# Performance work log

Measured on AMD Instinct MI355X. Metric: run time of the kernel, lower is better.

## Reference

```python
import jax, jax.numpy as jnp
import numpy as np

N_NEAR = 16
BN_EPS = 1e-5


def fps(xyz, n_center):
    # farthest point sampling, deterministic start at index 0. xyz: [B,N,C]
    B, N, _ = xyz.shape
    dist0 = jnp.full((B, N), jnp.inf, dtype=xyz.dtype)
    far0 = jnp.zeros((B,), dtype=jnp.int32)

    def step(carry, _):
        dist, far = carry
        centroid = jnp.take_along_axis(xyz, far[:, None, None], axis=1)  # [B,1,C]
        d = jnp.sum((xyz - centroid) ** 2, axis=-1)                       # [B,N]
        dist = jnp.minimum(dist, d)
        nxt = jnp.argmax(dist, axis=-1).astype(jnp.int32)
        return (dist, nxt), far

    _, idxs = jax.lax.scan(step, (dist0, far0), None, length=n_center)
    return jnp.transpose(idxs)  # [B, n_center]


def knn(xyz, k):
    # k nearest neighbors (self included), xyz: [B,N,C] -> idx [B,N,k]
    sq = jnp.sum(xyz * xyz, axis=-1)
    d = sq[:, :, None] - 2.0 * jnp.einsum('bnc,bmc->bnm', xyz, xyz) + sq[:, None, :]
    _, idx = jax.lax.top_k(-d, k)
    return idx


def gather_points(x, idx):
    # x: [B,N,...], idx: [B,*dims] int -> [B,*dims,...]
    return jax.vmap(lambda xb, ib: xb[ib])(x, idx)


def conv_bn_relu(x, W, b, g, be):
    # x: [B,C,K,S]; 1x1 Conv2d + BatchNorm2d (training/batch stats) + ReLU
    y = jnp.einsum('oc,bcks->boks', W, x) + b[None, :, None, None]
    mean = jnp.mean(y, axis=(0, 2, 3), keepdims=True)
    var = jnp.mean((y - mean) ** 2, axis=(0, 2, 3), keepdims=True)  # biased var, as torch BN
    y = (y - mean) * jax.lax.rsqrt(var + BN_EPS)
    y = y * g[None, :, None, None] + be[None, :, None, None]
    return jax.nn.relu(y)


def setup_inputs() -> dict:
    key = jax.random.key(0)
    ks = jax.random.split(key, 8)
    B, N, EMB = 16, 2048, 64
    mlp = [64, 128, 256]
    in_ch = 2 + EMB
    inp = {
        'xy': jax.random.normal(ks[0], (B, 2, N), dtype=jnp.float32),
        'fea': jax.random.normal(ks[1], (B, EMB, N), dtype=jnp.float32),
    }
    last = in_ch
    for i, out in enumerate(mlp):
        inp[f'W{i+1}'] = 0.1 * jax.random.normal(ks[2 + i], (out, last), dtype=jnp.float32)
        inp[f'b{i+1}'] = jnp.zeros((out,), dtype=jnp.float32)
        inp[f'g{i+1}'] = jnp.ones((out,), dtype=jnp.float32)
        inp[f'be{i+1}'] = jnp.zeros((out,), dtype=jnp.float32)
        last = out
    return inp


def reference(xy, fea, W1, b1, g1, be1, W2, b2, g2, be2, W3, b3, g3, be3):
    B, _, N = xy.shape
    n_center = N // 2 + 1
    xyz = jnp.transpose(xy, (0, 2, 1))   # [B,N,2]
    f = jnp.transpose(fea, (0, 2, 1))    # [B,N,emb]

    fps_idx = fps(xyz, n_center)                      # [B,S]
    new_xyz = gather_points(xyz, fps_idx)             # [B,S,2]
    knn_idx = knn(xyz, N_NEAR)                        # [B,N,k]
    knn_of_fps = gather_points(knn_idx, fps_idx)      # [B,S,k]
    grouped_xyz = gather_points(xyz, knn_of_fps)      # [B,S,k,2]
    grouped_norm = grouped_xyz - new_xyz[:, :, None, :]
    grouped_f = gather_points(f, knn_of_fps)          # [B,S,k,emb]
    new_fea = jnp.concatenate([grouped_norm, grouped_f], axis=-1)  # [B,S,k,C]

    x = jnp.transpose(new_fea, (0, 3, 2, 1))          # [B,C,k,S]
    for (W, b, g, be) in ((W1, b1, g1, be1), (W2, b2, g2, be2), (W3, b3, g3, be3)):
        x = conv_bn_relu(x, W, b, g, be)
    out = jnp.max(x, axis=2)                          # [B,C_out,S]
    return jnp.transpose(new_xyz, (0, 2, 1)), out
```

## Files before the change

kernel.cpp:

```cpp
#include <hip/hip_runtime.h>
#include <math.h>

#define B_   16
#define N_   2048
#define S_   1025
#define K_   16
#define EMB_ 64
#define NF_  (B_ * S_ * K_)
#define NCH_ (NF_ / 64)
#define NBS_ (NCH_ * 4)

typedef float v2f __attribute__((ext_vector_type(2)));
typedef short bf16x8 __attribute__((ext_vector_type(8)));
typedef float f32x4 __attribute__((ext_vector_type(4)));

__device__ __forceinline__ unsigned short f2bf(float f) {
  unsigned u = __float_as_uint(f);
  u += 0x7fffu + ((u >> 16) & 1u);
  return (unsigned short)(u >> 16);
}
__device__ __forceinline__ float bfl(unsigned pk) { return __uint_as_float((pk & 0xffffu) << 16); }
__device__ __forceinline__ float bfh(unsigned pk) { return __uint_as_float(pk & 0xffff0000u); }

__global__ __launch_bounds__(256) __attribute__((amdgpu_waves_per_eu(1, 1)))
void fps_pk_kernel(const float* __restrict__ xy, const float* __restrict__ fea,
                   const float* __restrict__ W1,
                   const float* __restrict__ W2, const float* __restrict__ W3,
                   int* __restrict__ fps_idx, float* __restrict__ new_xyz,
                   float* __restrict__ out0, unsigned* __restrict__ Pp,
                   unsigned short* __restrict__ W2b, unsigned short* __restrict__ W3b) {
  __shared__ float smem[8192];
  if (blockIdx.x < 16) {
    const int b = blockIdx.x;
    float2* lxy = reinterpret_cast<float2*>(smem);
    const int lane = threadIdx.x;
    const float* xb = xy + (size_t)b * 2 * N_;
    v2f pxp[16], pyp[16];
    float dist[32];
    if (lane < 64) {
      const float2* xb2 = (const float2*)xb;
      const float2* yb2 = (const float2*)(xb + N_);
#pragma unroll
      for (int q = 0; q < 16; ++q) {
        float2 x01 = xb2[lane * 16 + q];
        float2 y01 = yb2[lane * 16 + q];
        int p = lane * 32 + 2 * q;
        lxy[p] = make_float2(x01.x, y01.x);
        lxy[p + 1] = make_float2(x01.y, y01.y);
        pxp[q][0] = x01.x; pxp[q][1] = x01.y;
        pyp[q][0] = y01.x; pyp[q][1] = y01.y;
        dist[2 * q] = __builtin_inff();
        dist[2 * q + 1] = __builtin_inff();
      }
#pragma unroll
      for (int q = 0; q < 16; ++q) {
        asm volatile("" : "+v"(pxp[q]), "+v"(pyp[q]));
      }
    }
    __syncthreads();
    if (lane < 64) {
      int cur = 0;
      for (int t = 0; t < S_; ++t) {
        float2 c = lxy[cur];
        if (lane == 0) {
          fps_idx[b * S_ + t] = cur;
          new_xyz[(b * S_ + t) * 2 + 0] = c.x;
          new_xyz[(b * S_ + t) * 2 + 1] = c.y;
          out0[b * 2 * S_ + t] = c.x;
          out0[b * 2 * S_ + S_ + t] = c.y;
        }
        const float ncx = -c.x, ncy = -c.y;
        v2f ncx2; ncx2[0] = ncx; ncx2[1] = ncx;
        v2f ncy2; ncy2[0] = ncy; ncy2[1] = ncy;
#pragma unroll
        for (int q = 0; q < 16; ++q) {
          v2f dx, dy, sx, sy, dd;
          asm("v_pk_add_f32 %0, %1, %2" : "=v"(dx) : "v"(pxp[q]), "v"(ncx2));
          asm("v_pk_add_f32 %0, %1, %2" : "=v"(dy) : "v"(pyp[q]), "v"(ncy2));
          asm("v_pk_mul_f32 %0, %1, %1" : "=v"(sx) : "v"(dx));
          asm("v_pk_mul_f32 %0, %1, %1" : "=v"(sy) : "v"(dy));
          asm("v_pk_add_f32 %0, %1, %2" : "=v"(dd) : "v"(sx), "v"(sy));
          dist[2 * q] = fminf(dist[2 * q], dd[0]);
          dist[2 * q + 1] = fminf(dist[2 * q + 1], dd[1]);
        }
        float m1[16], m2[8], m3[4], m4[2];
#pragma unroll
        for (int j = 0; j < 16; ++j) m1[j] = fmaxf(dist[2 * j], dist[2 * j + 1]);
#pragma unroll
        for (int j = 0; j < 8; ++j) m2[j] = fmaxf(m1[2 * j], m1[2 * j + 1]);
#pragma unroll
        for (int j = 0; j < 4; ++j) m3[j] = fmaxf(m2[2 * j], m2[2 * j + 1]);
        m4[0] = fmaxf(m3[0], m3[1]);
        m4[1] = fmaxf(m3[2], m3[3]);
        const float lmax = fmaxf(m4[0], m4[1]);
        int xr = __float_as_int(lmax);
#define DPP_MAX_STEP(CTRL)                                                        \
        {                                                                         \
          int tmp_ = __builtin_amdgcn_update_dpp(xr, xr, (CTRL), 0xF, 0xF, false);\
          xr = __float_as_int(fmaxf(__int_as_float(xr), __int_as_float(tmp_)));   \
        }
        DPP_MAX_STEP(0x111)
        DPP_MAX_STEP(0x112)
        DPP_MAX_STEP(0x114)
        DPP_MAX_STEP(0x118)
        DPP_MAX_STEP(0x142)
        DPP_MAX_STEP(0x143)
#undef DPP_MAX_STEP
        const float g = __int_as_float(__builtin_amdgcn_readlane(xr, 63));
        int n = (m4[0] == g) ? 0 : 1;
        float c3 = (n & 1) ? m3[2] : m3[0];
        n = 2 * n + ((c3 == g) ? 0 : 1);
        float lo2 = (n & 1) ? m2[2] : m2[0];
        float hi2 = (n & 1) ? m2[6] : m2[4];
        float c2 = (n & 2) ? hi2 : lo2;
        n = 2 * n + ((c2 == g) ? 0 : 1);
        float a0 = (n & 1) ? m1[2] : m1[0];
        float a1 = (n & 1) ? m1[6] : m1[4];
        float a2 = (n & 1) ? m1[10] : m1[8];
        float a3 = (n & 1) ? m1[14] : m1[12];
        float b0 = (n & 2) ? a1 : a0;
        float b1 = (n & 2) ? a3 : a2;
        float c1 = (n & 4) ? b1 : b0;
        n = 2 * n + ((c1 == g) ? 0 : 1);
        float e0 = (n & 1) ? dist[2] : dist[0];
        float e1 = (n & 1) ? dist[6] : dist[4];
        float e2 = (n & 1) ? dist[10] : dist[8];
        float e3 = (n & 1) ? dist[14] : dist[12];
        float e4 = (n & 1) ? dist[18] : dist[16];
        float e5 = (n & 1) ? dist[22] : dist[20];
        float e6 = (n & 1) ? dist[26] : dist[24];
        float e7 = (n & 1) ? dist[30] : dist[28];
        float f0 = (n & 2) ? e1 : e0;
        float f1 = (n & 2) ? e3 : e2;
        float f2 = (n & 2) ? e5 : e4;
        float f3 = (n & 2) ? e7 : e6;
        float g0 = (n & 4) ? f1 : f0;
        float g1 = (n & 4) ? f3 : f2;
        float c0 = (n & 8) ? g1 : g0;
        const int lf = 2 * n + ((c0 == g) ? 0 : 1);
        unsigned long long mask = __ballot(lmax == g);
        int first = __ffsll(mask) - 1;
        cur = __builtin_amdgcn_readlane(lane * 32 + lf, first);
      }
    }
  } else if (blockIdx.x < 528) {
    const int bid = blockIdx.x - 16;
    const int t = threadIdx.x;
    const int b = bid >> 5;
    const int pt0 = (bid & 31) << 6;
    float* W1L = smem;
    float* feaL = smem + 4096;
#pragma unroll
    for (int p = 0; p < 16; ++p) {
      int idx = t + 256 * p;
      int c = idx >> 6, e = idx & 63;
      W1L[e * 64 + c] = W1[c * 66 + 2 + e];
      int r = (t >> 6) + 4 * p, cc = t & 63;
      feaL[r * 64 + cc] = fea[((size_t)b * 64 + r) * N_ + pt0 + cc];
    }
    __syncthreads();
    const int tpt = t & 15, tcq = t >> 4;
    float acc[4][4];
#pragma unroll
    for (int i = 0; i < 4; ++i)
#pragma unroll
      for (int j = 0; j < 4; ++j) acc[i][j] = 0.f;
    for (int e = 0; e < 64; ++e) {
      float4 a4 = *reinterpret_cast<const float4*>(&W1L[e * 64 + tcq * 4]);
      float4 b4 = *reinterpret_cast<const float4*>(&feaL[e * 64 + tpt * 4]);
      const float av[4] = {a4.x, a4.y, a4.z, a4.w};
      const float bvv[4] = {b4.x, b4.y, b4.z, b4.w};
#pragma unroll
      for (int i = 0; i < 4; ++i)
#pragma unroll
        for (int j = 0; j < 4; ++j) acc[i][j] = fmaf(av[i], bvv[j], acc[i][j]);
    }
#pragma unroll
    for (int j = 0; j < 4; ++j) {
      int pt = tpt * 4 + j;
      unsigned lo = (unsigned)f2bf(acc[0][j]) | ((unsigned)f2bf(acc[1][j]) << 16);
      unsigned hi = (unsigned)f2bf(acc[2][j]) | ((unsigned)f2bf(acc[3][j]) << 16);
      unsigned* dst = &Pp[((size_t)(b * N_ + pt0 + pt)) * 32 + tcq * 2];
      dst[0] = lo;
      dst[1] = hi;
    }
  } else {
    const int t = threadIdx.x;
    for (int i = t; i < 128 * 64; i += 256) W2b[i] = f2bf(W2[i]);
    for (int i = t; i < 256 * 128; i += 256) W3b[i] = f2bf(W3[i]);
  }
}

__global__ __launch_bounds__(256) void knn_kernel(const float* __restrict__ xy,
                                                  const int* __restrict__ fps_idx,
                                                  int* __restrict__ knn_sel) {
  const int b = blockIdx.y;
  __shared__ float2 lxy[N_];
  __shared__ double lsq[N_];
  const float* xb = xy + (size_t)b * 2 * N_;
  for (int p = threadIdx.x; p < N_; p += 256) {
    float x = xb[p], y = xb[N_ + p];
    lxy[p] = make_float2(x, y);
    lsq[p] = (double)x * (double)x + (double)y * (double)y;
  }
  __syncthreads();
  const int t = threadIdx.x;
  const int s = blockIdx.x * 8 + (t >> 5);
  if (s >= S_) return;
  const int oct = t & 31;
  const int p0 = fps_idx[b * S_ + s];
  float2 q = lxy[p0];
  const double xn = (double)q.x, yn = (double)q.y;
  const double sqn = lsq[p0];
  double d16[16];
  int i16[16];
#pragma unroll
  for (int j = 0; j < 16; ++j) { d16[j] = __builtin_inf(); i16[j] = 0x7fffffff; }
  const int mlo = oct * 64;
  for (int m0 = mlo; m0 < mlo + 64; m0 += 4) {
    double dd[4];
#pragma unroll
    for (int u = 0; u < 4; ++u) {
      float2 p = lxy[m0 + u];
      double dot = (double)p.x * xn + (double)p.y * yn;
      dd[u] = (sqn - 2.0 * dot) + lsq[m0 + u];
    }
#pragma unroll
    for (int u = 0; u < 4; ++u) {
      if (dd[u] < d16[15]) {
        double d = dd[u];
        int mi = m0 + u;
#pragma unroll
        for (int j = 15; j >= 1; --j) {
          bool shift = d < d16[j - 1];
          bool ins = d < d16[j];
          d16[j] = shift ? d16[j - 1] : (ins ? d : d16[j]);
          i16[j] = shift ? i16[j - 1] : (ins ? mi : i16[j]);
        }
        if (d < d16[0]) { d16[0] = d; i16[0] = mi; }
      }
    }
  }
#pragma unroll
  for (int w = 1; w <= 16; w <<= 1) {
    double nd[16]; int ni[16];
#pragma unroll
    for (int i = 0; i < 16; ++i) {
      double rd = __shfl_xor(d16[15 - i], w, 64);
      int ri = __shfl_xor(i16[15 - i], w, 64);
      bool takeR = (rd < d16[i]) || (rd == d16[i] && ri < i16[i]);
      nd[i] = takeR ? rd : d16[i];
      ni[i] = takeR ? ri : i16[i];
    }
#pragma unroll
    for (int i = 0; i < 16; ++i) { d16[i] = nd[i]; i16[i] = ni[i]; }
    if (w < 16) {
#pragma unroll
      for (int dstg = 8; dstg >= 1; dstg >>= 1) {
#pragma unroll
        for (int i = 0; i < 16; ++i) {
          if ((i & dstg) == 0) {
            int a = i, c = i + dstg;
            bool sw = (d16[a] > d16[c]) || (d16[a] == d16[c] && i16[a] > i16[c]);
            double tlo = sw ? d16[c] : d16[a];
            double thi = sw ? d16[a] : d16[c];
            int ulo = sw ? i16[c] : i16[a];
            int uhi = sw ? i16[a] : i16[c];
            d16[a] = tlo; d16[c] = thi; i16[a] = ulo; i16[c] = uhi;
          }
        }
      }
    }
  }
  if (oct == 0) {
    int* dst = knn_sel + ((size_t)b * S_ + s) * K_;
#pragma unroll
    for (int j = 0; j < 16; ++j) dst[j] = i16[j];
  }
}

__global__ __launch_bounds__(256) void yk1_kernel(const float* __restrict__ xy,
                                                  const int* __restrict__ knn_sel,
                                                  const float* __restrict__ new_xyz,
                                                  const unsigned* __restrict__ Pp,
                                                  const float* __restrict__ W1,
                                                  const float* __restrict__ b1,
                                                  unsigned* __restrict__ Y1p) {
  __shared__ float w0s[64], w1s[64], bbs[64];
  const int t = threadIdx.x;
  if (t < 64) { w0s[t] = W1[t * 66 + 0]; w1s[t] = W1[t * 66 + 1]; bbs[t] = b1[t]; }
  __syncthreads();
  const int n = blockIdx.x * 256 + t;
  const int bs = n >> 4;
  const int b = bs / S_;
  const int nbr = knn_sel[n];
  const float dx = xy[(size_t)b * 2 * N_ + nbr] - new_xyz[bs * 2 + 0];
  const float dy = xy[(size_t)b * 2 * N_ + N_ + nbr] - new_xyz[bs * 2 + 1];
  const unsigned* prow = &Pp[((size_t)(b * N_ + nbr)) * 32];
#pragma unroll 8
  for (int j = 0; j < 32; ++j) {
    unsigned pj = prow[j];
    int c = 2 * j;
    float v0 = bfl(pj) + w0s[c] * dx + w1s[c] * dy + bbs[c];
    float v1 = bfh(pj) + w0s[c + 1] * dx + w1s[c + 1] * dy + bbs[c + 1];
    Y1p[(size_t)j * NF_ + n] = (unsigned)f2bf(v0) | ((unsigned)f2bf(v1) << 16);
  }
}

__global__ __launch_bounds__(256) void rowstats_kernel(const unsigned* __restrict__ Y1p,
                                                       float* __restrict__ parts) {
  const int j = blockIdx.x & 31;
  const int seg = blockIdx.x >> 5;
  const int SEG = NF_ / 8;
  const unsigned* p = Y1p + (size_t)j * NF_ + (size_t)seg * SEG;
  double s0 = 0, q0 = 0, s1 = 0, q1 = 0;
  for (int i = threadIdx.x; i < SEG; i += 256) {
    unsigned pk = p[i];
    double a = (double)bfl(pk), b = (double)bfh(pk);
    s0 += a; q0 = fma(a, a, q0);
    s1 += b; q1 = fma(b, b, q1);
  }
  __shared__ double sh[4][256];
  sh[0][threadIdx.x] = s0; sh[1][threadIdx.x] = q0;
  sh[2][threadIdx.x] = s1; sh[3][threadIdx.x] = q1;
  __syncthreads();
  for (int o = 128; o > 0; o >>= 1) {
    if (threadIdx.x < o) {
#pragma unroll
      for (int u = 0; u < 4; ++u) sh[u][threadIdx.x] += sh[u][threadIdx.x + o];
    }
    __syncthreads();
  }
  if (threadIdx.x == 0) {
    float* dst = parts + (size_t)(j * 8 + seg) * 4;
    dst[0] = (float)sh[0][0];
    dst[1] = (float)sh[2][0];
    dst[2] = (float)sh[1][0];
    dst[3] = (float)sh[3][0];
  }
}

__global__ void redabsch1_kernel(const float* __restrict__ parts,
                                 const float* __restrict__ g, const float* __restrict__ be,
                                 float* __restrict__ A, float* __restrict__ D) {
  int m = threadIdx.x;
  if (m >= 64) return;
  int j = m >> 1, par = m & 1;
  double a = 0.0, b = 0.0;
  for (int seg = 0; seg < 8; ++seg) {
    const float* src = parts + (size_t)(j * 8 + seg) * 4;
    a += (double)src[par];
    b += (double)src[2 + par];
  }
  double mu = a * (1.0 / NF_);
  double var = b * (1.0 / NF_) - mu * mu;
  double aa = (double)g[m] / sqrt(var + 1e-5);
  A[m] = (float)aa;
  D[m] = (float)((double)be[m] - aa * mu);
}

__global__ void redabsch_kernel(const float* __restrict__ parts, int P, int M,
                                const float* __restrict__ g, const float* __restrict__ be,
                                float* __restrict__ A, float* __restrict__ D) {
  int m = threadIdx.x;
  if (m >= M) return;
  double a = 0.0, b = 0.0;
  for (int p = 0; p < P; ++p) {
    a += (double)parts[(size_t)p * 2 * M + m];
    b += (double)parts[(size_t)p * 2 * M + M + m];
  }
  double mu = a * (1.0 / NF_);
  double var = b * (1.0 / NF_) - mu * mu;
  double aa = (double)g[m] / sqrt(var + 1e-5);
  A[m] = (float)aa;
  D[m] = (float)((double)be[m] - aa * mu);
}

__device__ __forceinline__ float rowsum16(float v) {
#define RADD(CTRL) { int tm_ = __builtin_amdgcn_update_dpp(0, __float_as_int(v), (CTRL), 0xF, 0xF, true); \
                     v += __int_as_float(tm_); }
  RADD(0x111) RADD(0x112) RADD(0x114) RADD(0x118)
#undef RADD
  return v;
}

__device__ __forceinline__ void stage_x1(const unsigned* Y1p, const float* ab1, char* x1c,
                                         size_t n0, int w, int L) {
#pragma unroll
  for (int e = 0; e < 8; ++e) {
    int k0 = 2 * (w + 4 * e);
    unsigned pkv = Y1p[(size_t)(k0 >> 1) * NF_ + n0 + L];
    float v0 = fmaxf(fmaf(bfl(pkv), ab1[k0], ab1[64 + k0]), 0.f);
    float v1 = fmaxf(fmaf(bfh(pkv), ab1[k0 + 1], ab1[64 + k0 + 1]), 0.f);
    unsigned pk = (unsigned)f2bf(v0) | ((unsigned)f2bf(v1) << 16);
    *reinterpret_cast<unsigned*>(&x1c[L * 128 + ((2 * k0) ^ ((L & 7) << 4))]) = pk;
  }
}

__global__ __launch_bounds__(256) void passA_mfma_kernel(
    const unsigned* __restrict__ Y1p, const unsigned short* __restrict__ W2b,
    const float* __restrict__ A1v, const float* __restrict__ Bc1v,
    float* __restrict__ parts) {
  __shared__ float ab1[128];
  __shared__ __align__(16) unsigned short x1b[64 * 64];
  const int t = threadIdx.x;
  const int w = t >> 6, L = t & 63;
  if (t < 128) ab1[t] = (t < 64) ? A1v[t] : Bc1v[t - 64];
  bf16x8 w2f[2][2];
#pragma unroll
  for (int rb = 0; rb < 2; ++rb)
#pragma unroll
    for (int ks = 0; ks < 2; ++ks) {
      int row = (2 * w + rb) * 16 + (L & 15);
      int koff = ks * 32 + (L >> 4) * 8;
      w2f[rb][ks] = *reinterpret_cast<const bf16x8*>(&W2b[row * 64 + koff]);
    }
  float vs[2][4], vq[2][4];
#pragma unroll
  for (int rb = 0; rb < 2; ++rb)
#pragma unroll
    for (int r = 0; r < 4; ++r) { vs[rb][r] = 0.f; vq[rb][r] = 0.f; }
  char* x1c = reinterpret_cast<char*>(x1b);
  for (int ch = blockIdx.x; ch < NCH_; ch += 512) {
    const size_t n0 = (size_t)ch * 64;
    __syncthreads();
    stage_x1(Y1p, ab1, x1c, n0, w, L);
    __syncthreads();
#pragma unroll
    for (int rb = 0; rb < 2; ++rb) {
      f32x4 acc2[4];
#pragma unroll
      for (int cb = 0; cb < 4; ++cb) acc2[cb][0] = acc2[cb][1] = acc2[cb][2] = acc2[cb][3] = 0.f;
#pragma unroll
      for (int ks = 0; ks < 2; ++ks)
#pragma unroll
        for (int cb = 0; cb < 4; ++cb) {
          int n = cb * 16 + (L & 15);
          int koff = ks * 32 + (L >> 4) * 8;
          bf16x8 bfr = *reinterpret_cast<const bf16x8*>(&x1c[n * 128 + ((2 * koff) ^ ((n & 7) << 4))]);
          acc2[cb] = __builtin_amdgcn_mfma_f32_16x16x32_bf16(w2f[rb][ks], bfr, acc2[cb], 0, 0, 0);
        }
#pragma unroll
      for (int cb = 0; cb < 4; ++cb)
#pragma unroll
        for (int r = 0; r < 4; ++r) {
          float y = acc2[cb][r];
          vs[rb][r] += y;
          vq[rb][r] = fmaf(y, y, vq[rb][r]);
        }
    }
  }
#pragma unroll
  for (int rb = 0; rb < 2; ++rb)
#pragma unroll
    for (int r = 0; r < 4; ++r) {
      float s = rowsum16(vs[rb][r]);
      float q = rowsum16(vq[rb][r]);
      if ((L & 15) == 15) {
        int row = (2 * w + rb) * 16 + (L >> 4) * 4 + r;
        parts[(size_t)blockIdx.x * 256 + row] = s;
        parts[(size_t)blockIdx.x * 256 + 128 + row] = q;
      }
    }
}

__global__ __launch_bounds__(256) void passB_mfma_kernel(
    const unsigned* __restrict__ Y1p,
    const unsigned short* __restrict__ W2b, const unsigned short* __restrict__ W3b,
    const float* __restrict__ A1v, const float* __restrict__ Bc1v,
    const float* __restrict__ A2v, const float* __restrict__ D2v,
    float* __restrict__ parts, unsigned* __restrict__ M3) {
  __shared__ float ab1[128];
  __shared__ __align__(16) unsigned short x1b[64 * 64];
  __shared__ __align__(16) unsigned short x2b[64 * 128];
  const int t = threadIdx.x;
  const int w = t >> 6, L = t & 63;
  if (t < 128) ab1[t] = (t < 64) ? A1v[t] : Bc1v[t - 64];
  bf16x8 w3f[4][4];
#pragma unroll
  for (int rb = 0; rb < 4; ++rb)
#pragma unroll
    for (int ks = 0; ks < 4; ++ks) {
      int row = (4 * w + rb) * 16 + (L & 15);
      int koff = ks * 32 + (L >> 4) * 8;
      w3f[rb][ks] = *reinterpret_cast<const bf16x8*>(&W3b[row * 128 + koff]);
    }
  bf16x8 w2f[2][2];
#pragma unroll
  for (int rb = 0; rb < 2; ++rb)
#pragma unroll
    for (int ks = 0; ks < 2; ++ks) {
      int row = (2 * w + rb) * 16 + (L & 15);
      int koff = ks * 32 + (L >> 4) * 8;
      w2f[rb][ks] = *reinterpret_cast<const bf16x8*>(&W2b[row * 64 + koff]);
    }
  float vs[4][4], vq[4][4];
#pragma unroll
  for (int rb = 0; rb < 4; ++rb)
#pragma unroll
    for (int r = 0; r < 4; ++r) { vs[rb][r] = 0.f; vq[rb][r] = 0.f; }
  char* x1c = reinterpret_cast<char*>(x1b);
  char* x2c = reinterpret_cast<char*>(x2b);
  for (int ch = blockIdx.x; ch < NCH_; ch += 256) {
    const size_t n0 = (size_t)ch * 64;
    __syncthreads();
    stage_x1(Y1p, ab1, x1c, n0, w, L);
    __syncthreads();
#pragma unroll
    for (int rb = 0; rb < 2; ++rb) {
      f32x4 acc2[4];
#pragma unroll
      for (int cb = 0; cb < 4; ++cb) acc2[cb][0] = acc2[cb][1] = acc2[cb][2] = acc2[cb][3] = 0.f;
#pragma unroll
      for (int ks = 0; ks < 2; ++ks)
#pragma unroll
        for (int cb = 0; cb < 4; ++cb) {
          int n = cb * 16 + (L & 15);
          int koff = ks * 32 + (L >> 4) * 8;
          bf16x8 bfr = *reinterpret_cast<const bf16x8*>(&x1c[n * 128 + ((2 * koff) ^ ((n & 7) << 4))]);
          acc2[cb] = __builtin_amdgcn_mfma_f32_16x16x32_bf16(w2f[rb][ks], bfr, acc2[cb], 0, 0, 0);
        }
#pragma unroll
      for (int cb = 0; cb < 4; ++cb) {
        int n = cb * 16 + (L & 15);
        int kbase = (2 * w + rb) * 16 + (L >> 4) * 4;
#pragma unroll
        for (int rp = 0; rp < 2; ++rp) {
          int r0 = 2 * rp;
          float a0 = A2v[kbase + r0], d0 = D2v[kbase + r0];
          float a1 = A2v[kbase + r0 + 1], d1 = D2v[kbase + r0 + 1];
          float v0 = fmaxf(fmaf(acc2[cb][r0], a0, d0), 0.f);
          float v1 = fmaxf(fmaf(acc2[cb][r0 + 1], a1, d1), 0.f);
          unsigned pk = (unsigned)f2bf(v0) | ((unsigned)f2bf(v1) << 16);
          int k0 = kbase + r0;
          *reinterpret_cast<unsigned*>(&x2c[n * 256 + ((2 * k0) ^ ((n & 7) << 4))]) = pk;
        }
      }
    }
    __syncthreads();
    bf16x8 b3[4][4];
#pragma unroll
    for (int cb = 0; cb < 4; ++cb)
#pragma unroll
      for (int ks = 0; ks < 4; ++ks) {
        int n = cb * 16 + (L & 15);
        int koff = ks * 32 + (L >> 4) * 8;
        b3[cb][ks] = *reinterpret_cast<const bf16x8*>(&x2c[n * 256 + ((2 * koff) ^ ((n & 7) << 4))]);
      }
#pragma unroll
    for (int rb = 0; rb < 4; ++rb) {
      f32x4 acc3[4];
#pragma unroll
      for (int cb = 0; cb < 4; ++cb) acc3[cb][0] = acc3[cb][1] = acc3[cb][2] = acc3[cb][3] = 0.f;
#pragma unroll
      for (int ks = 0; ks < 4; ++ks)
#pragma unroll
        for (int cb = 0; cb < 4; ++cb)
          acc3[cb] = __builtin_amdgcn_mfma_f32_16x16x32_bf16(w3f[rb][ks], b3[cb][ks], acc3[cb], 0, 0, 0);
#pragma unroll
      for (int cb = 0; cb < 4; ++cb)
#pragma unroll
        for (int r = 0; r < 4; ++r) {
          float y = acc3[cb][r];
          vs[rb][r] += y;
          vq[rb][r] = fmaf(y, y, vq[rb][r]);
        }
      {
        int rowbase = (4 * w + rb) * 16 + (L >> 4) * 4;
#pragma unroll
        for (int cb = 0; cb < 4; ++cb) {
#pragma unroll
          for (int r = 0; r < 4; ++r) {
            float v = acc3[cb][r];
            int xi = __float_as_int(v), xm = __float_as_int(v);
#define RMAX(CTRL) { int tm_ = __builtin_amdgcn_update_dpp(xi, xi, (CTRL), 0xF, 0xF, false); \
                     xi = __float_as_int(fmaxf(__int_as_float(xi), __int_as_float(tm_))); }
#define RMIN(CTRL) { int tm_ = __builtin_amdgcn_update_dpp(xm, xm, (CTRL), 0xF, 0xF, false); \
                     xm = __float_as_int(fminf(__int_as_float(xm), __int_as_float(tm_))); }
            RMAX(0x111) RMAX(0x112) RMAX(0x114) RMAX(0x118)
            RMIN(0x111) RMIN(0x112) RMIN(0x114) RMIN(0x118)
#undef RMAX
#undef RMIN
            if ((L & 15) == 15) {
              int row = rowbase + r;
              int bs = ch * 4 + cb;
              M3[(size_t)row * NBS_ + bs] =
                  (unsigned)f2bf(__int_as_float(xi)) | ((unsigned)f2bf(__int_as_float(xm)) << 16);
            }
          }
        }
      }
    }
  }
#pragma unroll
  for (int rb = 0; rb < 4; ++rb)
#pragma unroll
    for (int r = 0; r < 4; ++r) {
      float s = rowsum16(vs[rb][r]);
      float q = rowsum16(vq[rb][r]);
      if ((L & 15) == 15) {
        int row = (4 * w + rb) * 16 + (L >> 4) * 4 + r;
        parts[(size_t)blockIdx.x * 512 + row] = s;
        parts[(size_t)blockIdx.x * 512 + 256 + row] = q;
      }
    }
}

__global__ __launch_bounds__(256) void final_small_kernel(
    const unsigned* __restrict__ M3, const float* __restrict__ A3,
    const float* __restrict__ D3, float* __restrict__ out1) {
  int gid = blockIdx.x * 256 + threadIdx.x;
  int row = gid / NBS_, bs = gid - row * NBS_;
  unsigned pk = M3[gid];
  float vmax = bfl(pk);
  float vmin = bfh(pk);
  float a = A3[row];
  float v = (a >= 0.f) ? vmax : vmin;
  int b = bs / S_, s = bs - b * S_;
  out1[((size_t)(b * 256 + row)) * S_ + s] = fmaxf(fmaf(v, a, D3[row]), 0.f);
}

__global__ void diag_kernel(float* out, float v) {
  if (threadIdx.x == 0 && blockIdx.x == 0) out[0] = v;
}

extern "C" void kernel_launch(void* const* d_in, const int* in_sizes, int n_in,
                              void* d_out, int out_size, void* d_ws, size_t ws_size,
                              hipStream_t stream) {
  const float* xy  = (const float*)d_in[0];
  const float* fea = (const float*)d_in[1];
  const float* W1  = (const float*)d_in[2];
  const float* b1  = (const float*)d_in[3];
  const float* g1  = (const float*)d_in[4];
  const float* be1 = (const float*)d_in[5];
  const float* W2  = (const float*)d_in[6];
  const float* g2  = (const float*)d_in[8];
  const float* be2 = (const float*)d_in[9];
  const float* W3  = (const float*)d_in[10];
  const float* g3  = (const float*)d_in[12];
  const float* be3 = (const float*)d_in[13];
  float* out = (float*)d_out;
  float* out1 = out + B_ * 2 * S_;

  char* w = (char*)d_ws;
  size_t off = 0;
  auto take = [&](size_t bytes) -> void* {
    void* p = w + off;
    off += (bytes + 255) & ~(size_t)255;
    return p;
  };
  int*      fps_idx = (int*)take((size_t)B_ * S_ * 4);
  float*    new_xyz = (float*)take((size_t)B_ * S_ * 2 * 4);
  int*      knn_sel = (int*)take((size_t)NF_ * 4);
  unsigned* Pp      = (unsigned*)take((size_t)B_ * N_ * 32 * 4);
  unsigned* Y1p     = (unsigned*)take((size_t)32 * NF_ * 4);
  float*    parts1  = (float*)take((size_t)256 * 4 * 4);
  float*    A1      = (float*)take(64 * 4);
  float*    Bc1     = (float*)take(64 * 4);
  float*    partsA  = (float*)take((size_t)512 * 256 * 4);
  float*    A2      = (float*)take(128 * 4);
  float*    D2      = (float*)take(128 * 4);
  float*    partsB  = (float*)take((size_t)256 * 512 * 4);
  float*    A3      = (float*)take(256 * 4);
  float*    D3      = (float*)take(256 * 4);
  unsigned short* W2b = (unsigned short*)take((size_t)128 * 64 * 2);
  unsigned short* W3b = (unsigned short*)take((size_t)256 * 128 * 2);
  unsigned* M3      = (unsigned*)take((size_t)256 * NBS_ * 4);

  if (off > ws_size) {
    diag_kernel<<<1, 64, 0, stream>>>(out, (float)(ws_size >> 20));
    return;
  }

  fps_pk_kernel<<<16 + 512 + 1, 256, 0, stream>>>(xy, fea, W1, W2, W3,
                                                  fps_idx, new_xyz, out, Pp, W2b, W3b);
  knn_kernel<<<dim3((S_ + 7) / 8, B_), 256, 0, stream>>>(xy, fps_idx, knn_sel);
  yk1_kernel<<<NF_ / 256, 256, 0, stream>>>(xy, knn_sel, new_xyz, Pp, W1, b1, Y1p);

  rowstats_kernel<<<256, 256, 0, stream>>>(Y1p, parts1);
  redabsch1_kernel<<<1, 64, 0, stream>>>(parts1, g1, be1, A1, Bc1);

  passA_mfma_kernel<<<512, 256, 0, stream>>>(Y1p, W2b, A1, Bc1, partsA);
  redabsch_kernel<<<1, 128, 0, stream>>>(partsA, 512, 128, g2, be2, A2, D2);

  passB_mfma_kernel<<<256, 256, 0, stream>>>(Y1p, W2b, W3b, A1, Bc1, A2, D2, partsB, M3);
  redabsch_kernel<<<1, 256, 0, stream>>>(partsB, 256, 256, g3, be3, A3, D3);

  final_small_kernel<<<(256 * NBS_) / 256, 256, 0, stream>>>(M3, A3, D3, out1);
}
```

Baseline: 1.351 ms.

## Fuse all stages into one persistent kernel with grid barriers and streamed FPS progress

Replaces the chain of ten separate launches with a single persistent 256-block kernel that uses atomic grid barriers between BN stages. The 16 FPS blocks publish per-batch progress, so the other blocks can pull KNN work items from an atomic queue and start on already-sampled centers while FPS is still running, after first draining the precompute work. This targets launch gaps and the serialization of KNN behind the long FPS loop. The risks are spin-wait overhead, the need for all 256 blocks to be co-resident to avoid deadlock, and reduced parallelism in later stages now capped at 256 blocks.

```diff
diff --git a/kernel.cpp b/kernel.cpp
--- a/kernel.cpp
+++ b/kernel.cpp
@@ -9,10 +9,18 @@
 #define NF_  (B_ * S_ * K_)
 #define NCH_ (NF_ / 64)
 #define NBS_ (NCH_ * 4)
+#define NBLK 256
+#define PK_UNITS 513
+#define KNN_ITEMS (129 * 16)
 
 typedef float v2f __attribute__((ext_vector_type(2)));
 typedef short bf16x8 __attribute__((ext_vector_type(8)));
 typedef float f32x4 __attribute__((ext_vector_type(4)));
+
+#define AL(p)    __hip_atomic_load((p), __ATOMIC_ACQUIRE, __HIP_MEMORY_SCOPE_AGENT)
+#define ALR(p)   __hip_atomic_load((p), __ATOMIC_RELAXED, __HIP_MEMORY_SCOPE_AGENT)
+#define ASR(p,v) __hip_atomic_store((p), (v), __ATOMIC_RELEASE, __HIP_MEMORY_SCOPE_AGENT)
+#define AADD(p)  __hip_atomic_fetch_add((p), 1, __ATOMIC_ACQ_REL, __HIP_MEMORY_SCOPE_AGENT)
 
 __device__ __forceinline__ unsigned short f2bf(float f) {
   unsigned u = __float_as_uint(f);
@@ -22,18 +30,67 @@
 __device__ __forceinline__ float bfl(unsigned pk) { return __uint_as_float((pk & 0xffffu) << 16); }
 __device__ __forceinline__ float bfh(unsigned pk) { return __uint_as_float(pk & 0xffff0000u); }
 
-__global__ __launch_bounds__(256) __attribute__((amdgpu_waves_per_eu(1, 1)))
-void fps_pk_kernel(const float* __restrict__ xy, const float* __restrict__ fea,
-                   const float* __restrict__ W1,
-                   const float* __restrict__ W2, const float* __restrict__ W3,
-                   int* __restrict__ fps_idx, float* __restrict__ new_xyz,
-                   float* __restrict__ out0, unsigned* __restrict__ Pp,
-                   unsigned short* __restrict__ W2b, unsigned short* __restrict__ W3b) {
-  __shared__ float smem[8192];
-  if (blockIdx.x < 16) {
-    const int b = blockIdx.x;
-    float2* lxy = reinterpret_cast<float2*>(smem);
-    const int lane = threadIdx.x;
+__device__ __forceinline__ float rowsum16(float v) {
+#define RADD(CTRL) { int tm_ = __builtin_amdgcn_update_dpp(0, __float_as_int(v), (CTRL), 0xF, 0xF, true); \
+                     v += __int_as_float(tm_); }
+  RADD(0x111) RADD(0x112) RADD(0x114) RADD(0x118)
+#undef RADD
+  return v;
+}
+
+__global__ void diag_kernel(float* out, float v) {
+  if (threadIdx.x == 0 && blockIdx.x == 0) out[0] = v;
+}
+
+__global__ __launch_bounds__(256, 1)
+void mega_kernel(const float* __restrict__ xy, const float* __restrict__ fea,
+                 const float* __restrict__ W1, const float* __restrict__ b1,
+                 const float* __restrict__ g1, const float* __restrict__ be1,
+                 const float* __restrict__ W2, const float* __restrict__ g2,
+                 const float* __restrict__ be2,
+                 const float* __restrict__ W3, const float* __restrict__ g3,
+                 const float* __restrict__ be3,
+                 int* fps_idx, float* new_xyz, int* knn_sel,
+                 unsigned* Pp, unsigned* Y1p, float* parts1,
+                 float* A1, float* Bc1, float* partsA, float* A2, float* D2,
+                 float* partsB, float* A3, float* D3,
+                 unsigned short* W2b, unsigned short* W3b, unsigned* M3,
+                 float* out0, float* out1, int* flags) {
+  __shared__ float2 sh_lxy[N_];
+  __shared__ double sh_lsq[N_];
+  __shared__ float sh_pkA[4096];
+  __shared__ float sh_pkB[4096];
+  __shared__ float sh_w0[64], sh_w1[64], sh_bb[64];
+  __shared__ double sh_red[4][256];
+  __shared__ float sh_ab1[128];
+  __shared__ __align__(16) unsigned short sh_x1b[64 * 64];
+  __shared__ __align__(16) unsigned short sh_x2b[64 * 128];
+  __shared__ int sh_unit;
+  __shared__ int sh_epoch;
+  const int bid = blockIdx.x;
+  const int tid = threadIdx.x;
+  int* progress = flags + 8;
+  if (tid == 0) sh_epoch = 0;
+  __syncthreads();
+
+  auto gbar = [&]() {
+    __syncthreads();
+    if (tid == 0) {
+      int my = ++sh_epoch;
+      int arrived = AADD(&flags[0]);
+      if (arrived == NBLK - 1) {
+        __hip_atomic_store(&flags[0], 0, __ATOMIC_RELAXED, __HIP_MEMORY_SCOPE_AGENT);
+        ASR(&flags[1], my);
+      } else {
+        while (AL(&flags[1]) < my) __builtin_amdgcn_s_sleep(8);
+      }
+    }
+    __syncthreads();
+  };
+
+  if (bid < 16) {
+    const int b = bid;
+    const int lane = tid;
     const float* xb = xy + (size_t)b * 2 * N_;
     v2f pxp[16], pyp[16];
     float dist[32];
@@ -45,8 +102,8 @@
         float2 x01 = xb2[lane * 16 + q];
         float2 y01 = yb2[lane * 16 + q];
         int p = lane * 32 + 2 * q;
-        lxy[p] = make_float2(x01.x, y01.x);
-        lxy[p + 1] = make_float2(x01.y, y01.y);
+        sh_lxy[p] = make_float2(x01.x, y01.x);
+        sh_lxy[p + 1] = make_float2(x01.y, y01.y);
         pxp[q][0] = x01.x; pxp[q][1] = x01.y;
         pyp[q][0] = y01.x; pyp[q][1] = y01.y;
         dist[2 * q] = __builtin_inff();
@@ -61,7 +118,7 @@
     if (lane < 64) {
       int cur = 0;
       for (int t = 0; t < S_; ++t) {
-        float2 c = lxy[cur];
+        float2 c = sh_lxy[cur];
         if (lane == 0) {
           fps_idx[b * S_ + t] = cur;
           new_xyz[(b * S_ + t) * 2 + 0] = c.x;
@@ -115,12 +172,12 @@
         float c2 = (n & 2) ? hi2 : lo2;
         n = 2 * n + ((c2 == g) ? 0 : 1);
         float a0 = (n & 1) ? m1[2] : m1[0];
-        float a1 = (n & 1) ? m1[6] : m1[4];
-        float a2 = (n & 1) ? m1[10] : m1[8];
-        float a3 = (n & 1) ? m1[14] : m1[12];
-        float b0 = (n & 2) ? a1 : a0;
-        float b1 = (n & 2) ? a3 : a2;
-        float c1 = (n & 4) ? b1 : b0;
+        float a1v = (n & 1) ? m1[6] : m1[4];
+        float a2v = (n & 1) ? m1[10] : m1[8];
+        float a3v = (n & 1) ? m1[14] : m1[12];
+        float b0 = (n & 2) ? a1v : a0;
+        float b1v = (n & 2) ? a3v : a2v;
+        float c1 = (n & 4) ? b1v : b0;
         n = 2 * n + ((c1 == g) ? 0 : 1);
         float e0 = (n & 1) ? dist[2] : dist[0];
         float e1 = (n & 1) ? dist[6] : dist[4];
@@ -135,493 +192,489 @@
         float f2 = (n & 2) ? e5 : e4;
         float f3 = (n & 2) ? e7 : e6;
         float g0 = (n & 4) ? f1 : f0;
-        float g1 = (n & 4) ? f3 : f2;
-        float c0 = (n & 8) ? g1 : g0;
+        float g1v = (n & 4) ? f3 : f2;
+        float c0 = (n & 8) ? g1v : g0;
         const int lf = 2 * n + ((c0 == g) ? 0 : 1);
         unsigned long long mask = __ballot(lmax == g);
         int first = __ffsll(mask) - 1;
         cur = __builtin_amdgcn_readlane(lane * 32 + lf, first);
-      }
-    }
-  } else if (blockIdx.x < 528) {
-    const int bid = blockIdx.x - 16;
-    const int t = threadIdx.x;
-    const int b = bid >> 5;
-    const int pt0 = (bid & 31) << 6;
-    float* W1L = smem;
-    float* feaL = smem + 4096;
-#pragma unroll
-    for (int p = 0; p < 16; ++p) {
-      int idx = t + 256 * p;
-      int c = idx >> 6, e = idx & 63;
-      W1L[e * 64 + c] = W1[c * 66 + 2 + e];
-      int r = (t >> 6) + 4 * p, cc = t & 63;
-      feaL[r * 64 + cc] = fea[((size_t)b * 64 + r) * N_ + pt0 + cc];
-    }
+        if (lane == 0 && ((t & 31) == 31 || t == S_ - 1)) {
+          ASR(&progress[b], t + 1);
+        }
+      }
+    }
+  } else {
+    for (;;) {
+      __syncthreads();
+      if (tid == 0) sh_unit = AADD(&flags[2]);
+      __syncthreads();
+      int u = sh_unit;
+      if (u >= PK_UNITS) break;
+      if (u < 512) {
+        const int b = u >> 5;
+        const int pt0 = (u & 31) << 6;
+#pragma unroll
+        for (int p = 0; p < 16; ++p) {
+          int idx = tid + 256 * p;
+          int c = idx >> 6, e = idx & 63;
+          sh_pkA[e * 64 + c] = W1[c * 66 + 2 + e];
+          int r = (tid >> 6) + 4 * p, cc = tid & 63;
+          sh_pkB[r * 64 + cc] = fea[((size_t)b * 64 + r) * N_ + pt0 + cc];
+        }
+        __syncthreads();
+        const int tpt = tid & 15, tcq = tid >> 4;
+        float acc[4][4];
+#pragma unroll
+        for (int i = 0; i < 4; ++i)
+#pragma unroll
+          for (int j = 0; j < 4; ++j) acc[i][j] = 0.f;
+        for (int e = 0; e < 64; ++e) {
+          float4 a4 = *reinterpret_cast<const float4*>(&sh_pkA[e * 64 + tcq * 4]);
+          float4 b4 = *reinterpret_cast<const float4*>(&sh_pkB[e * 64 + tpt * 4]);
+          const float av[4] = {a4.x, a4.y, a4.z, a4.w};
+          const float bvv[4] = {b4.x, b4.y, b4.z, b4.w};
+#pragma unroll
+          for (int i = 0; i < 4; ++i)
+#pragma unroll
+            for (int j = 0; j < 4; ++j) acc[i][j] = fmaf(av[i], bvv[j], acc[i][j]);
+        }
+#pragma unroll
+        for (int j = 0; j < 4; ++j) {
+          int pt = tpt * 4 + j;
+          unsigned lo = (unsigned)f2bf(acc[0][j]) | ((unsigned)f2bf(acc[1][j]) << 16);
+          unsigned hi = (unsigned)f2bf(acc[2][j]) | ((unsigned)f2bf(acc[3][j]) << 16);
+          unsigned* dst = &Pp[((size_t)(b * N_ + pt0 + pt)) * 32 + tcq * 2];
+          dst[0] = lo;
+          dst[1] = hi;
+        }
+      } else {
+        for (int i = tid; i < 128 * 64; i += 256) W2b[i] = f2bf(W2[i]);
+        for (int i = tid; i < 256 * 128; i += 256) W3b[i] = f2bf(W3[i]);
+      }
+    }
+    for (;;) {
+      __syncthreads();
+      if (tid == 0) sh_unit = AADD(&flags[4]);
+      __syncthreads();
+      int it = sh_unit;
+      if (it >= KNN_ITEMS) break;
+      const int b = it & 15;
+      const int s0 = (it >> 4) * 8;
+      const int sHi = (s0 + 8 < S_) ? (s0 + 8) : S_;
+      if (tid == 0) {
+        while (AL(&progress[b]) < sHi) __builtin_amdgcn_s_sleep(8);
+      }
+      __syncthreads();
+      const float* xb = xy + (size_t)b * 2 * N_;
+      for (int p = tid; p < N_; p += 256) {
+        float x = xb[p], y = xb[N_ + p];
+        sh_lxy[p] = make_float2(x, y);
+        sh_lsq[p] = (double)x * (double)x + (double)y * (double)y;
+      }
+      __syncthreads();
+      const int s = s0 + (tid >> 5);
+      const int oct = tid & 31;
+      if (s < S_) {
+        const int p0 = ALR((int*)&fps_idx[b * S_ + s]);
+        float2 q = sh_lxy[p0];
+        const double xn = (double)q.x, yn = (double)q.y;
+        const double sqn = sh_lsq[p0];
+        double d16[16];
+        int i16[16];
+#pragma unroll
+        for (int j = 0; j < 16; ++j) { d16[j] = __builtin_inf(); i16[j] = 0x7fffffff; }
+        const int mlo = oct * 64;
+        for (int m0 = mlo; m0 < mlo + 64; m0 += 4) {
+          double dd[4];
+#pragma unroll
+          for (int u2 = 0; u2 < 4; ++u2) {
+            float2 p = sh_lxy[m0 + u2];
+            double dot = (double)p.x * xn + (double)p.y * yn;
+            dd[u2] = (sqn - 2.0 * dot) + sh_lsq[m0 + u2];
+          }
+#pragma unroll
+          for (int u2 = 0; u2 < 4; ++u2) {
+            if (dd[u2] < d16[15]) {
+              double d = dd[u2];
+              int mi = m0 + u2;
+#pragma unroll
+              for (int j = 15; j >= 1; --j) {
+                bool shift = d < d16[j - 1];
+                bool ins = d < d16[j];
+                d16[j] = shift ? d16[j - 1] : (ins ? d : d16[j]);
+                i16[j] = shift ? i16[j - 1] : (ins ? mi : i16[j]);
+              }
+              if (d < d16[0]) { d16[0] = d; i16[0] = mi; }
+            }
+          }
+        }
+#pragma unroll
+        for (int w = 1; w <= 16; w <<= 1) {
+          double nd[16]; int ni[16];
+#pragma unroll
+          for (int i = 0; i < 16; ++i) {
+            double rd = __shfl_xor(d16[15 - i], w, 64);
+            int ri = __shfl_xor(i16[15 - i], w, 64);
+            bool takeR = (rd < d16[i]) || (rd == d16[i] && ri < i16[i]);
+            nd[i] = takeR ? rd : d16[i];
+            ni[i] = takeR ? ri : i16[i];
+          }
+#pragma unroll
+          for (int i = 0; i < 16; ++i) { d16[i] = nd[i]; i16[i] = ni[i]; }
+          if (w < 16) {
+#pragma unroll
+            for (int dstg = 8; dstg >= 1; dstg >>= 1) {
+#pragma unroll
+              for (int i = 0; i < 16; ++i) {
+                if ((i & dstg) == 0) {
+                  int a = i, c = i + dstg;
+                  bool sw = (d16[a] > d16[c]) || (d16[a] == d16[c] && i16[a] > i16[c]);
+                  double tlo = sw ? d16[c] : d16[a];
+                  double thi = sw ? d16[a] : d16[c];
+                  int ulo = sw ? i16[c] : i16[a];
+                  int uhi = sw ? i16[a] : i16[c];
+                  d16[a] = tlo; d16[c] = thi; i16[a] = ulo; i16[c] = uhi;
+                }
+              }
+            }
+          }
+        }
+        if (oct == 0) {
+          int* dst = knn_sel + ((size_t)b * S_ + s) * K_;
+#pragma unroll
+          for (int j = 0; j < 16; ++j) dst[j] = i16[j];
+        }
+      }
+    }
+  }
+
+  gbar();
+
+  if (tid < 64) { sh_w0[tid] = W1[tid * 66 + 0]; sh_w1[tid] = W1[tid * 66 + 1]; sh_bb[tid] = b1[tid]; }
+  __syncthreads();
+  for (int u = bid; u < NF_ / 256; u += NBLK) {
+    const int n = u * 256 + tid;
+    const int bs = n >> 4;
+    const int b = bs / S_;
+    const int nbr = knn_sel[n];
+    const float dx = xy[(size_t)b * 2 * N_ + nbr] - new_xyz[bs * 2 + 0];
+    const float dy = xy[(size_t)b * 2 * N_ + N_ + nbr] - new_xyz[bs * 2 + 1];
+    const unsigned* prow = &Pp[((size_t)(b * N_ + nbr)) * 32];
+#pragma unroll 8
+    for (int j = 0; j < 32; ++j) {
+      unsigned pj = prow[j];
+      int c = 2 * j;
+      float v0 = bfl(pj) + sh_w0[c] * dx + sh_w1[c] * dy + sh_bb[c];
+      float v1 = bfh(pj) + sh_w0[c + 1] * dx + sh_w1[c + 1] * dy + sh_bb[c + 1];
+      Y1p[(size_t)j * NF_ + n] = (unsigned)f2bf(v0) | ((unsigned)f2bf(v1) << 16);
+    }
+  }
+
+  gbar();
+
+  {
+    const int j = bid & 31;
+    const int seg = bid >> 5;
+    const int SEG = NF_ / 8;
+    const unsigned* p = Y1p + (size_t)j * NF_ + (size_t)seg * SEG;
+    double s0 = 0, q0 = 0, s1 = 0, q1 = 0;
+    for (int i = tid; i < SEG; i += 256) {
+      unsigned pk = p[i];
+      double a = (double)bfl(pk), b2 = (double)bfh(pk);
+      s0 += a; q0 = fma(a, a, q0);
+      s1 += b2; q1 = fma(b2, b2, q1);
+    }
+    sh_red[0][tid] = s0; sh_red[1][tid] = q0;
+    sh_red[2][tid] = s1; sh_red[3][tid] = q1;
     __syncthreads();
-    const int tpt = t & 15, tcq = t >> 4;
-    float acc[4][4];
-#pragma unroll
-    for (int i = 0; i < 4; ++i)
-#pragma unroll
-      for (int j = 0; j < 4; ++j) acc[i][j] = 0.f;
-    for (int e = 0; e < 64; ++e) {
-      float4 a4 = *reinterpret_cast<const float4*>(&W1L[e * 64 + tcq * 4]);
-      float4 b4 = *reinterpret_cast<const float4*>(&feaL[e * 64 + tpt * 4]);
-      const float av[4] = {a4.x, a4.y, a4.z, a4.w};
-      const float bvv[4] = {b4.x, b4.y, b4.z, b4.w};
-#pragma unroll
-      for (int i = 0; i < 4; ++i)
-#pragma unroll
-        for (int j = 0; j < 4; ++j) acc[i][j] = fmaf(av[i], bvv[j], acc[i][j]);
-    }
-#pragma unroll
-    for (int j = 0; j < 4; ++j) {
-      int pt = tpt * 4 + j;
-      unsigned lo = (unsigned)f2bf(acc[0][j]) | ((unsigned)f2bf(acc[1][j]) << 16);
-      unsigned hi = (unsigned)f2bf(acc[2][j]) | ((unsigned)f2bf(acc[3][j]) << 16);
-      unsigned* dst = &Pp[((size_t)(b * N_ + pt0 + pt)) * 32 + tcq * 2];
-      dst[0] = lo;
-      dst[1] = hi;
-    }
-  } else {
-    const int t = threadIdx.x;
-    for (int i = t; i < 128 * 64; i += 256) W2b[i] = f2bf(W2[i]);
-    for (int i = t; i < 256 * 128; i += 256) W3b[i] = f2bf(W3[i]);
-  }
-}
-
-__global__ __launch_bounds__(256) void knn_kernel(const float* __restrict__ xy,
-                                                  const int* __restrict__ fps_idx,
-                                                  int* __restrict__ knn_sel) {
-  const int b = blockIdx.y;
-  __shared__ float2 lxy[N_];
-  __shared__ double lsq[N_];
-  const float* xb = xy + (size_t)b * 2 * N_;
-  for (int p = threadIdx.x; p < N_; p += 256) {
-    float x = xb[p], y = xb[N_ + p];
-    lxy[p] = make_float2(x, y);
-    lsq[p] = (double)x * (double)x + (double)y * (double)y;
-  }
+    for (int o = 128; o > 0; o >>= 1) {
+      if (tid < o) {
+#pragma unroll
+        for (int u = 0; u < 4; ++u) sh_red[u][tid] += sh_red[u][tid + o];
+      }
+      __syncthreads();
+    }
+    if (tid == 0) {
+      float* dst = parts1 + (size_t)(j * 8 + seg) * 4;
+      dst[0] = (float)sh_red[0][0];
+      dst[1] = (float)sh_red[2][0];
+      dst[2] = (float)sh_red[1][0];
+      dst[3] = (float)sh_red[3][0];
+    }
+  }
+
+  gbar();
+
+  if (bid == 0 && tid < 64) {
+    int j = tid >> 1, par = tid & 1;
+    double a = 0.0, b2 = 0.0;
+    for (int seg = 0; seg < 8; ++seg) {
+      const float* src = parts1 + (size_t)(j * 8 + seg) * 4;
+      a += (double)src[par];
+      b2 += (double)src[2 + par];
+    }
+    double mu = a * (1.0 / NF_);
+    double var = b2 * (1.0 / NF_) - mu * mu;
+    double aa = (double)g1[tid] / sqrt(var + 1e-5);
+    A1[tid] = (float)aa;
+    Bc1[tid] = (float)((double)be1[tid] - aa * mu);
+  }
+
+  gbar();
+
+  const int w = tid >> 6, L = tid & 63;
+  char* x1c = reinterpret_cast<char*>(sh_x1b);
+  char* x2c = reinterpret_cast<char*>(sh_x2b);
+  if (tid < 128) sh_ab1[tid] = (tid < 64) ? A1[tid] : Bc1[tid - 64];
   __syncthreads();
-  const int t = threadIdx.x;
-  const int s = blockIdx.x * 8 + (t >> 5);
-  if (s >= S_) return;
-  const int oct = t & 31;
-  const int p0 = fps_idx[b * S_ + s];
-  float2 q = lxy[p0];
-  const double xn = (double)q.x, yn = (double)q.y;
-  const double sqn = lsq[p0];
-  double d16[16];
-  int i16[16];
-#pragma unroll
-  for (int j = 0; j < 16; ++j) { d16[j] = __builtin_inf(); i16[j] = 0x7fffffff; }
-  const int mlo = oct * 64;
-  for (int m0 = mlo; m0 < mlo + 64; m0 += 4) {
-    double dd[4];
-#pragma unroll
-    for (int u = 0; u < 4; ++u) {
-      float2 p = lxy[m0 + u];
-      double dot = (double)p.x * xn + (double)p.y * yn;
-      dd[u] = (sqn - 2.0 * dot) + lsq[m0 + u];
-    }
-#pragma unroll
-    for (int u = 0; u < 4; ++u) {
-      if (dd[u] < d16[15]) {
-        double d = dd[u];
-        int mi = m0 + u;
-#pragma unroll
-        for (int j = 15; j >= 1; --j) {
-          bool shift = d < d16[j - 1];
-          bool ins = d < d16[j];
-          d16[j] = shift ? d16[j - 1] : (ins ? d : d16[j]);
-          i16[j] = shift ? i16[j - 1] : (ins ? mi : i16[j]);
-        }
-        if (d < d16[0]) { d16[0] = d; i16[0] = mi; }
-      }
-    }
-  }
-#pragma unroll
-  for (int w = 1; w <= 16; w <<= 1) {
-    double nd[16]; int ni[16];
-#pragma unroll
-    for (int i = 0; i < 16; ++i) {
-      double rd = __shfl_xor(d16[15 - i], w, 64);
-      int ri = __shfl_xor(i16[15 - i], w, 64);
-      bool takeR = (rd < d16[i]) || (rd == d16[i] && ri < i16[i]);
-      nd[i] = takeR ? rd : d16[i];
-      ni[i] = takeR ? ri : i16[i];
-    }
-#pragma unroll
-    for (int i = 0; i < 16; ++i) { d16[i] = nd[i]; i16[i] = ni[i]; }
-    if (w < 16) {
-#pragma unroll
-      for (int dstg = 8; dstg >= 1; dstg >>= 1) {
-#pragma unroll
-        for (int i = 0; i < 16; ++i) {
-          if ((i & dstg) == 0) {
-            int a = i, c = i + dstg;
-            bool sw = (d16[a] > d16[c]) || (d16[a] == d16[c] && i16[a] > i16[c]);
-            double tlo = sw ? d16[c] : d16[a];
-            double thi = sw ? d16[a] : d16[c];
-            int ulo = sw ? i16[c] : i16[a];
-            int uhi = sw ? i16[a] : i16[c];
-            d16[a] = tlo; d16[c] = thi; i16[a] = ulo; i16[c] = uhi;
-          }
-        }
-      }
-    }
-  }
-  if (oct == 0) {
-    int* dst = knn_sel + ((size_t)b * S_ + s) * K_;
-#pragma unroll
-    for (int j = 0; j < 16; ++j) dst[j] = i16[j];
-  }
-}
-
-__global__ __launch_bounds__(256) void yk1_kernel(const float* __restrict__ xy,
-                                                  const int* __restrict__ knn_sel,
-                                                  const float* __restrict__ new_xyz,
-                                                  const unsigned* __restrict__ Pp,
-                                                  const float* __restrict__ W1,
-                                                  const float* __restrict__ b1,
-                                                  unsigned* __restrict__ Y1p) {
-  __shared__ float w0s[64], w1s[64], bbs[64];
-  const int t = threadIdx.x;
-  if (t < 64) { w0s[t] = W1[t * 66 + 0]; w1s[t] = W1[t * 66 + 1]; bbs[t] = b1[t]; }
-  __syncthreads();
-  const int n = blockIdx.x * 256 + t;
-  const int bs = n >> 4;
-  const int b = bs / S_;
-  const int nbr = knn_sel[n];
-  const float dx = xy[(size_t)b * 2 * N_ + nbr] - new_xyz[bs * 2 + 0];
-  const float dy = xy[(size_t)b * 2 * N_ + N_ + nbr] - new_xyz[bs * 2 + 1];
-  const unsigned* prow = &Pp[((size_t)(b * N_ + nbr)) * 32];
-#pragma unroll 8
-  for (int j = 0; j < 32; ++j) {
-    unsigned pj = prow[j];
-    int c = 2 * j;
-    float v0 = bfl(pj) + w0s[c] * dx + w1s[c] * dy + bbs[c];
-    float v1 = bfh(pj) + w0s[c + 1] * dx + w1s[c + 1] * dy + bbs[c + 1];
-    Y1p[(size_t)j * NF_ + n] = (unsigned)f2bf(v0) | ((unsigned)f2bf(v1) << 16);
-  }
-}
-
-__global__ __launch_bounds__(256) void rowstats_kernel(const unsigned* __restrict__ Y1p,
-                                                       float* __restrict__ parts) {
-  const int j = blockIdx.x & 31;
-  const int seg = blockIdx.x >> 5;
-  const int SEG = NF_ / 8;
-  const unsigned* p = Y1p + (size_t)j * NF_ + (size_t)seg * SEG;
-  double s0 = 0, q0 = 0, s1 = 0, q1 = 0;
-  for (int i = threadIdx.x; i < SEG; i += 256) {
-    unsigned pk = p[i];
-    double a = (double)bfl(pk), b = (double)bfh(pk);
-    s0 += a; q0 = fma(a, a, q0);
-    s1 += b; q1 = fma(b, b, q1);
-  }
-  __shared__ double sh[4][256];
-  sh[0][threadIdx.x] = s0; sh[1][threadIdx.x] = q0;
-  sh[2][threadIdx.x] = s1; sh[3][threadIdx.x] = q1;
-  __syncthreads();
-  for (int o = 128; o > 0; o >>= 1) {
-    if (threadIdx.x < o) {
-#pragma unroll
-      for (int u = 0; u < 4; ++u) sh[u][threadIdx.x] += sh[u][threadIdx.x + o];
-    }
-    __syncthreads();
-  }
-  if (threadIdx.x == 0) {
-    float* dst = parts + (size_t)(j * 8 + seg) * 4;
-    dst[0] = (float)sh[0][0];
-    dst[1] = (float)sh[2][0];
-    dst[2] = (float)sh[1][0];
-    dst[3] = (float)sh[3][0];
-  }
-}
-
-__global__ void redabsch1_kernel(const float* __restrict__ parts,
-                                 const float* __restrict__ g, const float* __restrict__ be,
-                                 float* __restrict__ A, float* __restrict__ D) {
-  int m = threadIdx.x;
-  if (m >= 64) return;
-  int j = m >> 1, par = m & 1;
-  double a = 0.0, b = 0.0;
-  for (int seg = 0; seg < 8; ++seg) {
-    const float* src = parts + (size_t)(j * 8 + seg) * 4;
-    a += (double)src[par];
-    b += (double)src[2 + par];
-  }
-  double mu = a * (1.0 / NF_);
-  double var = b * (1.0 / NF_) - mu * mu;
-  double aa = (double)g[m] / sqrt(var + 1e-5);
-  A[m] = (float)aa;
-  D[m] = (float)((double)be[m] - aa * mu);
-}
-
-__global__ void redabsch_kernel(const float* __restrict__ parts, int P, int M,
-                                const float* __restrict__ g, const float* __restrict__ be,
-                                float* __restrict__ A, float* __restrict__ D) {
-  int m = threadIdx.x;
-  if (m >= M) return;
-  double a = 0.0, b = 0.0;
-  for (int p = 0; p < P; ++p) {
-    a += (double)parts[(size_t)p * 2 * M + m];
-    b += (double)parts[(size_t)p * 2 * M + M + m];
-  }
-  double mu = a * (1.0 / NF_);
-  double var = b * (1.0 / NF_) - mu * mu;
-  double aa = (double)g[m] / sqrt(var + 1e-5);
-  A[m] = (float)aa;
-  D[m] = (float)((double)be[m] - aa * mu);
-}
-
-__device__ __forceinline__ float rowsum16(float v) {
-#define RADD(CTRL) { int tm_ = __builtin_amdgcn_update_dpp(0, __float_as_int(v), (CTRL), 0xF, 0xF, true); \
-                     v += __int_as_float(tm_); }
-  RADD(0x111) RADD(0x112) RADD(0x114) RADD(0x118)
-#undef RADD
-  return v;
-}
-
-__device__ __forceinline__ void stage_x1(const unsigned* Y1p, const float* ab1, char* x1c,
-                                         size_t n0, int w, int L) {
-#pragma unroll
-  for (int e = 0; e < 8; ++e) {
-    int k0 = 2 * (w + 4 * e);
-    unsigned pkv = Y1p[(size_t)(k0 >> 1) * NF_ + n0 + L];
-    float v0 = fmaxf(fmaf(bfl(pkv), ab1[k0], ab1[64 + k0]), 0.f);
-    float v1 = fmaxf(fmaf(bfh(pkv), ab1[k0 + 1], ab1[64 + k0 + 1]), 0.f);
-    unsigned pk = (unsigned)f2bf(v0) | ((unsigned)f2bf(v1) << 16);
-    *reinterpret_cast<unsigned*>(&x1c[L * 128 + ((2 * k0) ^ ((L & 7) << 4))]) = pk;
-  }
-}
-
-__global__ __launch_bounds__(256) void passA_mfma_kernel(
-    const unsigned* __restrict__ Y1p, const unsigned short* __restrict__ W2b,
-    const float* __restrict__ A1v, const float* __restrict__ Bc1v,
-    float* __restrict__ parts) {
-  __shared__ float ab1[128];
-  __shared__ __align__(16) unsigned short x1b[64 * 64];
-  const int t = threadIdx.x;
-  const int w = t >> 6, L = t & 63;
-  if (t < 128) ab1[t] = (t < 64) ? A1v[t] : Bc1v[t - 64];
-  bf16x8 w2f[2][2];
-#pragma unroll
-  for (int rb = 0; rb < 2; ++rb)
-#pragma unroll
-    for (int ks = 0; ks < 2; ++ks) {
-      int row = (2 * w + rb) * 16 + (L & 15);
-      int koff = ks * 32 + (L >> 4) * 8;
-      w2f[rb][ks] = *reinterpret_cast<const bf16x8*>(&W2b[row * 64 + koff]);
-    }
-  float vs[2][4], vq[2][4];
-#pragma unroll
-  for (int rb = 0; rb < 2; ++rb)
-#pragma unroll
-    for (int r = 0; r < 4; ++r) { vs[rb][r] = 0.f; vq[rb][r] = 0.f; }
-  char* x1c = reinterpret_cast<char*>(x1b);
-  for (int ch = blockIdx.x; ch < NCH_; ch += 512) {
-    const size_t n0 = (size_t)ch * 64;
-    __syncthreads();
-    stage_x1(Y1p, ab1, x1c, n0, w, L);
-    __syncthreads();
-#pragma unroll
-    for (int rb = 0; rb < 2; ++rb) {
-      f32x4 acc2[4];
-#pragma unroll
-      for (int cb = 0; cb < 4; ++cb) acc2[cb][0] = acc2[cb][1] = acc2[cb][2] = acc2[cb][3] = 0.f;
-#pragma unroll
-      for (int ks = 0; ks < 2; ++ks)
+
+  {
+    bf16x8 w2f[2][2];
+#pragma unroll
+    for (int rb = 0; rb < 2; ++rb)
+#pragma unroll
+      for (int ks = 0; ks < 2; ++ks) {
+        int row = (2 * w + rb) * 16 + (L & 15);
+        int koff = ks * 32 + (L >> 4) * 8;
+        w2f[rb][ks] = *reinterpret_cast<const bf16x8*>(&W2b[row * 64 + koff]);
+      }
+    float vs[2][4], vq[2][4];
+#pragma unroll
+    for (int rb = 0; rb < 2; ++rb)
+#pragma unroll
+      for (int r = 0; r < 4; ++r) { vs[rb][r] = 0.f; vq[rb][r] = 0.f; }
+    for (int ch = bid; ch < NCH_; ch += NBLK) {
+      const size_t n0 = (size_t)ch * 64;
+      __syncthreads();
+#pragma unroll
+      for (int e = 0; e < 8; ++e) {
+        int k0 = 2 * (w + 4 * e);
+        unsigned pkv = Y1p[(size_t)(k0 >> 1) * NF_ + n0 + L];
+        float v0 = fmaxf(fmaf(bfl(pkv), sh_ab1[k0], sh_ab1[64 + k0]), 0.f);
+        float v1 = fmaxf(fmaf(bfh(pkv), sh_ab1[k0 + 1], sh_ab1[64 + k0 + 1]), 0.f);
+        unsigned pk = (unsigned)f2bf(v0) | ((unsigned)f2bf(v1) << 16);
+        *reinterpret_cast<unsigned*>(&x1c[L * 128 + ((2 * k0) ^ ((L & 7) << 4))]) = pk;
+      }
+      __syncthreads();
+#pragma unroll
+      for (int rb = 0; rb < 2; ++rb) {
+        f32x4 acc2[4];
+#pragma unroll
+        for (int cb = 0; cb < 4; ++cb) acc2[cb][0] = acc2[cb][1] = acc2[cb][2] = acc2[cb][3] = 0.f;
+#pragma unroll
+        for (int ks = 0; ks < 2; ++ks)
+#pragma unroll
+          for (int cb = 0; cb < 4; ++cb) {
+            int n = cb * 16 + (L & 15);
+            int koff = ks * 32 + (L >> 4) * 8;
+            bf16x8 bfr = *reinterpret_cast<const bf16x8*>(&x1c[n * 128 + ((2 * koff) ^ ((n & 7) << 4))]);
+            acc2[cb] = __builtin_amdgcn_mfma_f32_16x16x32_bf16(w2f[rb][ks], bfr, acc2[cb], 0, 0, 0);
+          }
+#pragma unroll
+        for (int cb = 0; cb < 4; ++cb)
+#pragma unroll
+          for (int r = 0; r < 4; ++r) {
+            float y = acc2[cb][r];
+            vs[rb][r] += y;
+            vq[rb][r] = fmaf(y, y, vq[rb][r]);
+          }
+      }
+    }
+#pragma unroll
+    for (int rb = 0; rb < 2; ++rb)
+#pragma unroll
+      for (int r = 0; r < 4; ++r) {
+        float s = rowsum16(vs[rb][r]);
+        float q = rowsum16(vq[rb][r]);
+        if ((L & 15) == 15) {
+          int row = (2 * w + rb) * 16 + (L >> 4) * 4 + r;
+          partsA[(size_t)bid * 256 + row] = s;
+          partsA[(size_t)bid * 256 + 128 + row] = q;
+        }
+      }
+  }
+
+  gbar();
+
+  if (bid == 0 && tid < 128) {
+    double a = 0.0, b2 = 0.0;
+    for (int p = 0; p < NBLK; ++p) {
+      a += (double)partsA[(size_t)p * 256 + tid];
+      b2 += (double)partsA[(size_t)p * 256 + 128 + tid];
+    }
+    double mu = a * (1.0 / NF_);
+    double var = b2 * (1.0 / NF_) - mu * mu;
+    double aa = (double)g2[tid] / sqrt(var + 1e-5);
+    A2[tid] = (float)aa;
+    D2[tid] = (float)((double)be2[tid] - aa * mu);
+  }
+
+  gbar();
+
+  {
+    bf16x8 w3f[4][4];
+#pragma unroll
+    for (int rb = 0; rb < 4; ++rb)
+#pragma unroll
+      for (int ks = 0; ks < 4; ++ks) {
+        int row = (4 * w + rb) * 16 + (L & 15);
+        int koff = ks * 32 + (L >> 4) * 8;
+        w3f[rb][ks] = *reinterpret_cast<const bf16x8*>(&W3b[row * 128 + koff]);
+      }
+    bf16x8 w2f[2][2];
+#pragma unroll
+    for (int rb = 0; rb < 2; ++rb)
+#pragma unroll
+      for (int ks = 0; ks < 2; ++ks) {
+        int row = (2 * w + rb) * 16 + (L & 15);
+        int koff = ks * 32 + (L >> 4) * 8;
+        w2f[rb][ks] = *reinterpret_cast<const bf16x8*>(&W2b[row * 64 + koff]);
+      }
+    float vs[4][4], vq[4][4];
+#pragma unroll
+    for (int rb = 0; rb < 4; ++rb)
+#pragma unroll
+      for (int r = 0; r < 4; ++r) { vs[rb][r] = 0.f; vq[rb][r] = 0.f; }
+    for (int ch = bid; ch < NCH_; ch += NBLK) {
+      const size_t n0 = (size_t)ch * 64;
+      __syncthreads();
+#pragma unroll
+      for (int e = 0; e < 8; ++e) {
+        int k0 = 2 * (w + 4 * e);
+        unsigned pkv = Y1p[(size_t)(k0 >> 1) * NF_ + n0 + L];
+        float v0 = fmaxf(fmaf(bfl(pkv), sh_ab1[k0], sh_ab1[64 + k0]), 0.f);
+        float v1 = fmaxf(fmaf(bfh(pkv), sh_ab1[k0 + 1], sh_ab1[64 + k0 + 1]), 0.f);
+        unsigned pk = (unsigned)f2bf(v0) | ((unsigned)f2bf(v1) << 16);
+        *reinterpret_cast<unsigned*>(&x1c[L * 128 + ((2 * k0) ^ ((L & 7) << 4))]) = pk;
+      }
+      __syncthreads();
+#pragma unroll
+      for (int rb = 0; rb < 2; ++rb) {
+        f32x4 acc2[4];
+#pragma unroll
+        for (int cb = 0; cb < 4; ++cb) acc2[cb][0] = acc2[cb][1] = acc2[cb][2] = acc2[cb][3] = 0.f;
+#pragma unroll
+        for (int ks = 0; ks < 2; ++ks)
+#pragma unroll
+          for (int cb = 0; cb < 4; ++cb) {
+            int n = cb * 16 + (L & 15);
+            int koff = ks * 32 + (L >> 4) * 8;
+            bf16x8 bfr = *reinterpret_cast<const bf16x8*>(&x1c[n * 128 + ((2 * koff) ^ ((n & 7) << 4))]);
+            acc2[cb] = __builtin_amdgcn_mfma_f32_16x16x32_bf16(w2f[rb][ks], bfr, acc2[cb], 0, 0, 0);
+          }
 #pragma unroll
         for (int cb = 0; cb < 4; ++cb) {
           int n = cb * 16 + (L & 15);
-          int koff = ks * 32 + (L >> 4) * 8;
-          bf16x8 bfr = *reinterpret_cast<const bf16x8*>(&x1c[n * 128 + ((2 * koff) ^ ((n & 7) << 4))]);
-          acc2[cb] = __builtin_amdgcn_mfma_f32_16x16x32_bf16(w2f[rb][ks], bfr, acc2[cb], 0, 0, 0);
-        }
+          int kbase = (2 * w + rb) * 16 + (L >> 4) * 4;
+#pragma unroll
+          for (int rp = 0; rp < 2; ++rp) {
+            int r0 = 2 * rp;
+            float a0 = A2[kbase + r0], d0 = D2[kbase + r0];
+            float a1 = A2[kbase + r0 + 1], d1 = D2[kbase + r0 + 1];
+            float v0 = fmaxf(fmaf(acc2[cb][r0], a0, d0), 0.f);
+            float v1 = fmaxf(fmaf(acc2[cb][r0 + 1], a1, d1), 0.f);
+            unsigned pk = (unsigned)f2bf(v0) | ((unsigned)f2bf(v1) << 16);
+            int k0 = kbase + r0;
+            *reinterpret_cast<unsigned*>(&x2c[n * 256 + ((2 * k0) ^ ((n & 7) << 4))]) = pk;
+          }
+        }
+      }
+      __syncthreads();
+      bf16x8 b3[4][4];
 #pragma unroll
       for (int cb = 0; cb < 4; ++cb)
 #pragma unroll
-        for (int r = 0; r < 4; ++r) {
-          float y = acc2[cb][r];
-          vs[rb][r] += y;
-          vq[rb][r] = fmaf(y, y, vq[rb][r]);
-        }
-    }
-  }
-#pragma unroll
-  for (int rb = 0; rb < 2; ++rb)
-#pragma unroll
-    for (int r = 0; r < 4; ++r) {
-      float s = rowsum16(vs[rb][r]);
-      float q = rowsum16(vq[rb][r]);
-      if ((L & 15) == 15) {
-        int row = (2 * w + rb) * 16 + (L >> 4) * 4 + r;
-        parts[(size_t)blockIdx.x * 256 + row] = s;
-        parts[(size_t)blockIdx.x * 256 + 128 + row] = q;
-      }
-    }
-}
-
-__global__ __launch_bounds__(256) void passB_mfma_kernel(
-    const unsigned* __restrict__ Y1p,
-    const unsigned short* __restrict__ W2b, const unsigned short* __restrict__ W3b,
-    const float* __restrict__ A1v, const float* __restrict__ Bc1v,
-    const float* __restrict__ A2v, const float* __restrict__ D2v,
-    float* __restrict__ parts, unsigned* __restrict__ M3) {
-  __shared__ float ab1[128];
-  __shared__ __align__(16) unsigned short x1b[64 * 64];
-  __shared__ __align__(16) unsigned short x2b[64 * 128];
-  const int t = threadIdx.x;
-  const int w = t >> 6, L = t & 63;
-  if (t < 128) ab1[t] = (t < 64) ? A1v[t] : Bc1v[t - 64];
-  bf16x8 w3f[4][4];
-#pragma unroll
-  for (int rb = 0; rb < 4; ++rb)
-#pragma unroll
-    for (int ks = 0; ks < 4; ++ks) {
-      int row = (4 * w + rb) * 16 + (L & 15);
-      int koff = ks * 32 + (L >> 4) * 8;
-      w3f[rb][ks] = *reinterpret_cast<const bf16x8*>(&W3b[row * 128 + koff]);
-    }
-  bf16x8 w2f[2][2];
-#pragma unroll
-  for (int rb = 0; rb < 2; ++rb)
-#pragma unroll
-    for (int ks = 0; ks < 2; ++ks) {
-      int row = (2 * w + rb) * 16 + (L & 15);
-      int koff = ks * 32 + (L >> 4) * 8;
-      w2f[rb][ks] = *reinterpret_cast<const bf16x8*>(&W2b[row * 64 + koff]);
-    }
-  float vs[4][4], vq[4][4];
-#pragma unroll
-  for (int rb = 0; rb < 4; ++rb)
-#pragma unroll
-    for (int r = 0; r < 4; ++r) { vs[rb][r] = 0.f; vq[rb][r] = 0.f; }
-  char* x1c = reinterpret_cast<char*>(x1b);
-  char* x2c = reinterpret_cast<char*>(x2b);
-  for (int ch = blockIdx.x; ch < NCH_; ch += 256) {
-    const size_t n0 = (size_t)ch * 64;
-    __syncthreads();
-    stage_x1(Y1p, ab1, x1c, n0, w, L);
-    __syncthreads();
-#pragma unroll
-    for (int rb = 0; rb < 2; ++rb) {
-      f32x4 acc2[4];
-#pragma unroll
-      for (int cb = 0; cb < 4; ++cb) acc2[cb][0] = acc2[cb][1] = acc2[cb][2] = acc2[cb][3] = 0.f;
-#pragma unroll
-      for (int ks = 0; ks < 2; ++ks)
-#pragma unroll
-        for (int cb = 0; cb < 4; ++cb) {
+        for (int ks = 0; ks < 4; ++ks) {
           int n = cb * 16 + (L & 15);
           int koff = ks * 32 + (L >> 4) * 8;
-          bf16x8 bfr = *reinterpret_cast<const bf16x8*>(&x1c[n * 128 + ((2 * koff) ^ ((n & 7) << 4))]);
-          acc2[cb] = __builtin_amdgcn_mfma_f32_16x16x32_bf16(w2f[rb][ks], bfr, acc2[cb], 0, 0, 0);
-        }
-#pragma unroll
-      for (int cb = 0; cb < 4; ++cb) {
-        int n = cb * 16 + (L & 15);
-        int kbase = (2 * w + rb) * 16 + (L >> 4) * 4;
-#pragma unroll
-        for (int rp = 0; rp < 2; ++rp) {
-          int r0 = 2 * rp;
-          float a0 = A2v[kbase + r0], d0 = D2v[kbase + r0];
-          float a1 = A2v[kbase + r0 + 1], d1 = D2v[kbase + r0 + 1];
-          float v0 = fmaxf(fmaf(acc2[cb][r0], a0, d0), 0.f);
-          float v1 = fmaxf(fmaf(acc2[cb][r0 + 1], a1, d1), 0.f);
-          unsigned pk = (unsigned)f2bf(v0) | ((unsigned)f2bf(v1) << 16);
-          int k0 = kbase + r0;
-          *reinterpret_cast<unsigned*>(&x2c[n * 256 + ((2 * k0) ^ ((n & 7) << 4))]) = pk;
-        }
-      }
-    }
-    __syncthreads();
-    bf16x8 b3[4][4];
-#pragma unroll
-    for (int cb = 0; cb < 4; ++cb)
-#pragma unroll
-      for (int ks = 0; ks < 4; ++ks) {
-        int n = cb * 16 + (L & 15);
-        int koff = ks * 32 + (L >> 4) * 8;
-        b3[cb][ks] = *reinterpret_cast<const bf16x8*>(&x2c[n * 256 + ((2 * koff) ^ ((n & 7) << 4))]);
-      }
-#pragma unroll
-    for (int rb = 0; rb < 4; ++rb) {
-      f32x4 acc3[4];
-#pragma unroll
-      for (int cb = 0; cb < 4; ++cb) acc3[cb][0] = acc3[cb][1] = acc3[cb][2] = acc3[cb][3] = 0.f;
-#pragma unroll
-      for (int ks = 0; ks < 4; ++ks)
+          b3[cb][ks] = *reinterpret_cast<const bf16x8*>(&x2c[n * 256 + ((2 * koff) ^ ((n & 7) << 4))]);
+        }
+#pragma unroll
+      for (int rb = 0; rb < 4; ++rb) {
+        f32x4 acc3[4];
+#pragma unroll
+        for (int cb = 0; cb < 4; ++cb) acc3[cb][0] = acc3[cb][1] = acc3[cb][2] = acc3[cb][3] = 0.f;
+#pragma unroll
+        for (int ks = 0; ks < 4; ++ks)
+#pragma unroll
+          for (int cb = 0; cb < 4; ++cb)
+            acc3[cb] = __builtin_amdgcn_mfma_f32_16x16x32_bf16(w3f[rb][ks], b3[cb][ks], acc3[cb], 0, 0, 0);
 #pragma unroll
         for (int cb = 0; cb < 4; ++cb)
-          acc3[cb] = __builtin_amdgcn_mfma_f32_16x16x32_bf16(w3f[rb][ks], b3[cb][ks], acc3[cb], 0, 0, 0);
-#pragma unroll
-      for (int cb = 0; cb < 4; ++cb)
-#pragma unroll
-        for (int r = 0; r < 4; ++r) {
-          float y = acc3[cb][r];
-          vs[rb][r] += y;
-          vq[rb][r] = fmaf(y, y, vq[rb][r]);
-        }
-      {
-        int rowbase = (4 * w + rb) * 16 + (L >> 4) * 4;
-#pragma unroll
-        for (int cb = 0; cb < 4; ++cb) {
 #pragma unroll
           for (int r = 0; r < 4; ++r) {
-            float v = acc3[cb][r];
-            int xi = __float_as_int(v), xm = __float_as_int(v);
+            float y = acc3[cb][r];
+            vs[rb][r] += y;
+            vq[rb][r] = fmaf(y, y, vq[rb][r]);
+          }
+        {
+          int rowbase = (4 * w + rb) * 16 + (L >> 4) * 4;
+#pragma unroll
+          for (int cb = 0; cb < 4; ++cb) {
+#pragma unroll
+            for (int r = 0; r < 4; ++r) {
+              float v = acc3[cb][r];
+              int xi = __float_as_int(v), xm = __float_as_int(v);
 #define RMAX(CTRL) { int tm_ = __builtin_amdgcn_update_dpp(xi, xi, (CTRL), 0xF, 0xF, false); \
                      xi = __float_as_int(fmaxf(__int_as_float(xi), __int_as_float(tm_))); }
 #define RMIN(CTRL) { int tm_ = __builtin_amdgcn_update_dpp(xm, xm, (CTRL), 0xF, 0xF, false); \
                      xm = __float_as_int(fminf(__int_as_float(xm), __int_as_float(tm_))); }
-            RMAX(0x111) RMAX(0x112) RMAX(0x114) RMAX(0x118)
-            RMIN(0x111) RMIN(0x112) RMIN(0x114) RMIN(0x118)
+              RMAX(0x111) RMAX(0x112) RMAX(0x114) RMAX(0x118)
+              RMIN(0x111) RMIN(0x112) RMIN(0x114) RMIN(0x118)
 #undef RMAX
 #undef RMIN
-            if ((L & 15) == 15) {
-              int row = rowbase + r;
-              int bs = ch * 4 + cb;
-              M3[(size_t)row * NBS_ + bs] =
-                  (unsigned)f2bf(__int_as_float(xi)) | ((unsigned)f2bf(__int_as_float(xm)) << 16);
+              if ((L & 15) == 15) {
+                int row = rowbase + r;
+                int bs = ch * 4 + cb;
+                M3[(size_t)row * NBS_ + bs] =
+                    (unsigned)f2bf(__int_as_float(xi)) | ((unsigned)f2bf(__int_as_float(xm)) << 16);
+              }
             }
           }
         }
       }
     }
-  }
-#pragma unroll
-  for (int rb = 0; rb < 4; ++rb)
-#pragma unroll
-    for (int r = 0; r < 4; ++r) {
-      float s = rowsum16(vs[rb][r]);
-      float q = rowsum16(vq[rb][r]);
-      if ((L & 15) == 15) {
-        int row = (4 * w + rb) * 16 + (L >> 4) * 4 + r;
-        parts[(size_t)blockIdx.x * 512 + row] = s;
-        parts[(size_t)blockIdx.x * 512 + 256 + row] = q;
-      }
-    }
-}
-
-__global__ __launch_bounds__(256) void final_small_kernel(
-    const unsigned* __restrict__ M3, const float* __restrict__ A3,
-    const float* __restrict__ D3, float* __restrict__ out1) {
-  int gid = blockIdx.x * 256 + threadIdx.x;
-  int row = gid / NBS_, bs = gid - row * NBS_;
-  unsigned pk = M3[gid];
-  float vmax = bfl(pk);
-  float vmin = bfh(pk);
-  float a = A3[row];
-  float v = (a >= 0.f) ? vmax : vmin;
-  int b = bs / S_, s = bs - b * S_;
-  out1[((size_t)(b * 256 + row)) * S_ + s] = fmaxf(fmaf(v, a, D3[row]), 0.f);
-}
-
-__global__ void diag_kernel(float* out, float v) {
-  if (threadIdx.x == 0 && blockIdx.x == 0) out[0] = v;
+#pragma unroll
+    for (int rb = 0; rb < 4; ++rb)
+#pragma unroll
+      for (int r = 0; r < 4; ++r) {
+        float s = rowsum16(vs[rb][r]);
+        float q = rowsum16(vq[rb][r]);
+        if ((L & 15) == 15) {
+          int row = (4 * w + rb) * 16 + (L >> 4) * 4 + r;
+          partsB[(size_t)bid * 512 + row] = s;
+          partsB[(size_t)bid * 512 + 256 + row] = q;
+        }
+      }
+  }
+
+  gbar();
+
+  if (bid == 0 && tid < 256) {
+    double a = 0.0, b2 = 0.0;
+    for (int p = 0; p < NBLK; ++p) {
+      a += (double)partsB[(size_t)p * 512 + tid];
+      b2 += (double)partsB[(size_t)p * 512 + 256 + tid];
+    }
+    double mu = a * (1.0 / NF_);
+    double var = b2 * (1.0 / NF_) - mu * mu;
+    double aa = (double)g3[tid] / sqrt(var + 1e-5);
+    A3[tid] = (float)aa;
+    D3[tid] = (float)((double)be3[tid] - aa * mu);
+  }
+
+  gbar();
+
+  for (int gid = bid * 256 + tid; gid < 256 * NBS_; gid += NBLK * 256) {
+    int row = gid / NBS_, bs = gid - row * NBS_;
+    unsigned pk = M3[gid];
+    float vmax = bfl(pk);
+    float vmin = bfh(pk);
+    float a = A3[row];
+    float v = (a >= 0.f) ? vmax : vmin;
+    int b = bs / S_, s = bs - b * S_;
+    out1[((size_t)(b * 256 + row)) * S_ + s] = fmaxf(fmaf(v, a, D3[row]), 0.f);
+  }
 }
 
 extern "C" void kernel_launch(void* const* d_in, const int* in_sizes, int n_in,
@@ -649,6 +702,7 @@
     off += (bytes + 255) & ~(size_t)255;
     return p;
   };
+  int*      flags   = (int*)take(256);
   int*      fps_idx = (int*)take((size_t)B_ * S_ * 4);
   float*    new_xyz = (float*)take((size_t)B_ * S_ * 2 * 4);
   int*      knn_sel = (int*)take((size_t)NF_ * 4);
@@ -657,10 +711,10 @@
   float*    parts1  = (float*)take((size_t)256 * 4 * 4);
   float*    A1      = (float*)take(64 * 4);
   float*    Bc1     = (float*)take(64 * 4);
-  float*    partsA  = (float*)take((size_t)512 * 256 * 4);
+  float*    partsA  = (float*)take((size_t)NBLK * 256 * 4);
   float*    A2      = (float*)take(128 * 4);
   float*    D2      = (float*)take(128 * 4);
-  float*    partsB  = (float*)take((size_t)256 * 512 * 4);
+  float*    partsB  = (float*)take((size_t)NBLK * 512 * 4);
   float*    A3      = (float*)take(256 * 4);
   float*    D3      = (float*)take(256 * 4);
   unsigned short* W2b = (unsigned short*)take((size_t)128 * 64 * 2);
@@ -672,19 +726,9 @@
     return;
   }
 
-  fps_pk_kernel<<<16 + 512 + 1, 256, 0, stream>>>(xy, fea, W1, W2, W3,
-                                                  fps_idx, new_xyz, out, Pp, W2b, W3b);
-  knn_kernel<<<dim3((S_ + 7) / 8, B_), 256, 0, stream>>>(xy, fps_idx, knn_sel);
-  yk1_kernel<<<NF_ / 256, 256, 0, stream>>>(xy, knn_sel, new_xyz, Pp, W1, b1, Y1p);
-
-  rowstats_kernel<<<256, 256, 0, stream>>>(Y1p, parts1);
-  redabsch1_kernel<<<1, 64, 0, stream>>>(parts1, g1, be1, A1, Bc1);
-
-  passA_mfma_kernel<<<512, 256, 0, stream>>>(Y1p, W2b, A1, Bc1, partsA);
-  redabsch_kernel<<<1, 128, 0, stream>>>(partsA, 512, 128, g2, be2, A2, D2);
-
-  passB_mfma_kernel<<<256, 256, 0, stream>>>(Y1p, W2b, W3b, A1, Bc1, A2, D2, partsB, M3);
-  redabsch_kernel<<<1, 256, 0, stream>>>(partsB, 256, 256, g3, be3, A3, D3);
-
-  final_small_kernel<<<(256 * NBS_) / 256, 256, 0, stream>>>(M3, A3, D3, out1);
+  hipMemsetAsync(flags, 0, 256, stream);
+  mega_kernel<<<NBLK, 256, 0, stream>>>(xy, fea, W1, b1, g1, be1, W2, g2, be2,
+                                        W3, g3, be3, fps_idx, new_xyz, knn_sel,
+                                        Pp, Y1p, parts1, A1, Bc1, partsA, A2, D2,
+                                        partsB, A3, D3, W2b, W3b, M3, out, out1, flags);
 }
```

Result: no change. 1.371 ms (+1.5%).
